# Performance work log

Hardware: AMD Instinct MI355X
Metric: run time of the kernel (lower is better)

Reference implementation:

```python
import jax, jax.numpy as jnp
import numpy as np
from functools import partial

L, B, E, H, NL = 512, 16, 768, 12, 12
D = E // H  # head dim = 64
FF = 4 * E
LN_EPS = 1e-5


def gelu_new(x):
    # HF openai-gpt ACT_FNS['gelu'] (tanh approximation)
    c = np.sqrt(2.0 / np.pi).astype(np.float32)
    return 0.5 * x * (1.0 + jnp.tanh(c * (x + 0.044715 * x * x * x)))


def layer_norm(x, g, b):
    mu = jnp.mean(x, axis=-1, keepdims=True)
    var = jnp.mean(jnp.square(x - mu), axis=-1, keepdims=True)
    return (x - mu) * jax.lax.rsqrt(var + LN_EPS) * g + b


def setup_inputs() -> dict:
    key = jax.random.key(0)
    ks = jax.random.split(key, 8)
    s = 0.02
    x = jax.random.normal(ks[0], (L, B, E), dtype=jnp.float32)
    custom_mask = jnp.ones((B, L), dtype=jnp.float32)
    pos_emb = s * jax.random.normal(ks[1], (L, E), dtype=jnp.float32)
    # stacked per-layer params (leading axis = layer)
    params = {
        'c_attn_w': s * jax.random.normal(ks[2], (NL, E, 3 * E), dtype=jnp.float32),
        'c_attn_b': jnp.zeros((NL, 3 * E), dtype=jnp.float32),
        'attn_proj_w': s * jax.random.normal(ks[3], (NL, E, E), dtype=jnp.float32),
        'attn_proj_b': jnp.zeros((NL, E), dtype=jnp.float32),
        'ln1_g': jnp.ones((NL, E), dtype=jnp.float32),
        'ln1_b': jnp.zeros((NL, E), dtype=jnp.float32),
        'c_fc_w': s * jax.random.normal(ks[4], (NL, E, FF), dtype=jnp.float32),
        'c_fc_b': jnp.zeros((NL, FF), dtype=jnp.float32),
        'mlp_proj_w': s * jax.random.normal(ks[5], (NL, FF, E), dtype=jnp.float32),
        'mlp_proj_b': jnp.zeros((NL, E), dtype=jnp.float32),
        'ln2_g': jnp.ones((NL, E), dtype=jnp.float32),
        'ln2_b': jnp.zeros((NL, E), dtype=jnp.float32),
    }
    return {'x': x, 'custom_mask': custom_mask, 'pos_emb': pos_emb, **params}


def _gpt_forward(x, custom_mask, pos_emb, c_attn_w, c_attn_b, attn_proj_w,
                 attn_proj_b, ln1_g, ln1_b, c_fc_w, c_fc_b, mlp_proj_w,
                 mlp_proj_b, ln2_g, ln2_b):
    Lx, Bx, Ex = x.shape
    h = x.transpose(1, 0, 2) + pos_emb[None, :Lx]  # (B, L, E); dropout = eval identity
    # additive padding mask: (1 - m) * finfo.min, broadcast over heads/queries
    add_mask = (1.0 - custom_mask)[:, None, None, :] * jnp.finfo(jnp.float32).min
    causal = jnp.tril(jnp.ones((Lx, Lx), dtype=jnp.float32))  # bias buffer b

    def block(h, p):
        (caw, cab, apw, apb, g1, b1, fw, fb, pw, pb, g2, b2) = p
        qkv = h @ caw + cab                              # (B, L, 3E)
        q, k, v = jnp.split(qkv, 3, axis=-1)
        q = q.reshape(Bx, Lx, H, D).transpose(0, 2, 1, 3)  # (B, H, L, D)
        k = k.reshape(Bx, Lx, H, D).transpose(0, 2, 1, 3)
        v = v.reshape(Bx, Lx, H, D).transpose(0, 2, 1, 3)
        w = jnp.einsum('bhqd,bhkd->bhqk', q, k) / np.float32(np.sqrt(D))
        w = w * causal + (-10000.0) * (1.0 - causal)     # causal bias masking
        w = w + add_mask
        a = jax.nn.softmax(w, axis=-1)
        o = jnp.einsum('bhqk,bhkd->bhqd', a, v)          # (B, H, L, D)
        o = o.transpose(0, 2, 1, 3).reshape(Bx, Lx, Ex)
        a_out = o @ apw + apb
        n = layer_norm(h + a_out, g1, b1)
        m = gelu_new(n @ fw + fb) @ pw + pb
        h2 = layer_norm(n + m, g2, b2)
        return h2, None

    params = (c_attn_w, c_attn_b, attn_proj_w, attn_proj_b, ln1_g, ln1_b,
              c_fc_w, c_fc_b, mlp_proj_w, mlp_proj_b, ln2_g, ln2_b)
    h, _ = jax.lax.scan(block, h, params)
    return h.transpose(1, 0, 2)  # back to (L, B, E)


def reference(x, custom_mask, pos_emb, c_attn_w, c_attn_b, attn_proj_w,
              attn_proj_b, ln1_g, ln1_b, c_fc_w, c_fc_b, mlp_proj_w,
              mlp_proj_b, ln2_g, ln2_b):
    return _gpt_forward(x, custom_mask, pos_emb, c_attn_w, c_attn_b,
                        attn_proj_w, attn_proj_b, ln1_g, ln1_b, c_fc_w,
                        c_fc_b, mlp_proj_w, mlp_proj_b, ln2_g, ln2_b)
```

## Files before the change

### kernel.cpp

```cpp
#include <hip/hip_runtime.h>
#include <cstdint>
#include <cstddef>


#define LSEQ 512
#define NBATCH 16
#define EDIM 768
#define NHEAD 12
#define NLAYER 12

typedef __attribute__((ext_vector_type(8))) short short8;
typedef __attribute__((ext_vector_type(4))) short short4v;
typedef __attribute__((ext_vector_type(4))) float f32x4;

__device__ __forceinline__ short f2bf(float f) {
  union { float f; unsigned u; } x; x.f = f;
  return (short)((x.u + 0x7FFFu + ((x.u >> 16) & 1u)) >> 16);
}
__device__ __forceinline__ float bf2f(short s) {
  union { unsigned u; float f; } x; x.u = ((unsigned)(unsigned short)s) << 16;
  return x.f;
}

__device__ __forceinline__ void gload_lds16(const void* g, void* l) {
  __builtin_amdgcn_global_load_lds(
      (__attribute__((address_space(1))) void*)(void*)g,
      (__attribute__((address_space(3))) void*)l, 16, 0, 0);
}

__global__ __launch_bounds__(256) void wt_transpose(const float* __restrict__ W,
                                                    short* __restrict__ Wt,
                                                    int K, int N) {
  __shared__ float tile[32][33];
  const int n0 = blockIdx.x * 32, k0 = blockIdx.y * 32;
  const size_t lo = (size_t)blockIdx.z * K * N;
  const float* Ws = W + lo;
  short* Wd = Wt + lo;
  const int tx = threadIdx.x & 31, ty = threadIdx.x >> 5;
#pragma unroll
  for (int i = 0; i < 4; ++i)
    tile[ty + i * 8][tx] = Ws[(size_t)(k0 + ty + i * 8) * N + n0 + tx];
  __syncthreads();
#pragma unroll
  for (int i = 0; i < 4; ++i)
    Wd[(size_t)(n0 + ty + i * 8) * K + k0 + tx] = f2bf(tile[tx][ty + i * 8]);
}

__global__ __launch_bounds__(256) void embed_k(const float* __restrict__ x,
                                               const float* __restrict__ pos,
                                               float* __restrict__ h,
                                               short* __restrict__ hbf) {
  const int row = blockIdx.x;
  const int b = row >> 9, lp = row & 511;
  const int t = threadIdx.x;
#pragma unroll
  for (int i = 0; i < 3; ++i) {
    const int e = t + i * 256;
    float v = x[(size_t)(lp * 16 + b) * 768 + e] + pos[(size_t)lp * 768 + e];
    h[(size_t)row * 768 + e] = v;
    hbf[(size_t)row * 768 + e] = f2bf(v);
  }
}

template <int FINAL>
__global__ __launch_bounds__(256) void ln_fused(const float* __restrict__ A,
                                                const short* __restrict__ B0,
                                                const short* __restrict__ B1,
                                                const float* __restrict__ g,
                                                const float* __restrict__ be,
                                                float* __restrict__ outf,
                                                short* __restrict__ outb) {
  const int row = blockIdx.x * 4 + (threadIdx.x >> 6);
  const int l = threadIdx.x & 63;
  const size_t base = (size_t)row * 768;
  float v[12];
  float s1 = 0.f, s2 = 0.f;
#pragma unroll
  for (int j = 0; j < 3; ++j) {
    const int e = j * 256 + l * 4;
    f32x4 a = *(const f32x4*)&A[base + e];
    short4v b0 = *(const short4v*)&B0[base + e];
    short4v b1 = *(const short4v*)&B1[base + e];
#pragma unroll
    for (int q = 0; q < 4; ++q) {
      float x = a[q] + bf2f(b0[q]) + bf2f(b1[q]);
      v[j * 4 + q] = x; s1 += x; s2 += x * x;
    }
  }
#pragma unroll
  for (int m = 1; m < 64; m <<= 1) {
    s1 += __shfl_xor(s1, m);
    s2 += __shfl_xor(s2, m);
  }
  const float mu = s1 * (1.f / 768.f);
  const float rs = rsqrtf(s2 * (1.f / 768.f) - mu * mu + 1e-5f);
  size_t obase = base;
  if constexpr (FINAL) {
    const int b = row >> 9, lp = row & 511;
    obase = (size_t)(lp * 16 + b) * 768;
  }
#pragma unroll
  for (int j = 0; j < 3; ++j) {
    const int e = j * 256 + l * 4;
    f32x4 gv = *(const f32x4*)&g[e];
    f32x4 bv = *(const f32x4*)&be[e];
    f32x4 of; short4v ob;
#pragma unroll
    for (int q = 0; q < 4; ++q) {
      float o = (v[j * 4 + q] - mu) * rs * gv[q] + bv[q];
      of[q] = o; ob[q] = f2bf(o);
    }
    *(f32x4*)&outf[obase + e] = of;
    if constexpr (!FINAL) *(short4v*)&outb[obase + e] = ob;
  }
}

template <int EPI>
__global__ __launch_bounds__(256) void gemm256(const short* __restrict__ A,
                                               const short* __restrict__ Bt,
                                               const float* __restrict__ bias,
                                               short* __restrict__ C,
                                               int N, int K) {
  constexpr int BK = 64;
  __shared__ alignas(16) short Alds[64 * BK];
  __shared__ alignas(16) short Blds[256 * BK];
  const int t = threadIdx.x;
  const int w = t >> 6, l = t & 63;
  const int wc = w;
  const int l15 = l & 15, lhi = l >> 4;
  const int rowA0 = blockIdx.x * 64;
  const int rowB0 = blockIdx.y * 256;

  f32x4 acc[4][4];
#pragma unroll
  for (int mi = 0; mi < 4; ++mi)
#pragma unroll
    for (int ni = 0; ni < 4; ++ni) acc[mi][ni] = (f32x4){0.f, 0.f, 0.f, 0.f};

  const int srl = w * 8 + (l >> 3);
  const int ss = l & 7;

  const short* aptr[2];
#pragma unroll
  for (int i = 0; i < 2; ++i) {
    const int r = i * 32 + srl;
    aptr[i] = A + (size_t)(rowA0 + r) * K + ((ss ^ (r & 7)) << 3);
  }
  const short* bptr[8];
#pragma unroll
  for (int i = 0; i < 8; ++i) {
    const int r = i * 32 + srl;
    bptr[i] = Bt + (size_t)(rowB0 + r) * K + ((ss ^ (r & 7)) << 3);
  }

  for (int kt = 0; kt < K; kt += BK) {
#pragma unroll
    for (int i = 0; i < 2; ++i) {
      gload_lds16(aptr[i], &Alds[(i * 32 + w * 8) * BK]);
      aptr[i] += BK;
    }
#pragma unroll
    for (int i = 0; i < 8; ++i) {
      gload_lds16(bptr[i], &Blds[(i * 32 + w * 8) * BK]);
      bptr[i] += BK;
    }
    __syncthreads();
    short8 af[4][2], bfr[4][2];
#pragma unroll
    for (int mi = 0; mi < 4; ++mi) {
      const int r = mi * 16 + l15;
#pragma unroll
      for (int kc = 0; kc < 2; ++kc)
        af[mi][kc] = *(const short8*)
            &Alds[r * BK + ((((kc << 2) | lhi) ^ (r & 7)) << 3)];
    }
#pragma unroll
    for (int ni = 0; ni < 4; ++ni) {
      const int r = wc * 64 + ni * 16 + l15;
#pragma unroll
      for (int kc = 0; kc < 2; ++kc)
        bfr[ni][kc] = *(const short8*)
            &Blds[r * BK + ((((kc << 2) | lhi) ^ (r & 7)) << 3)];
    }
#pragma unroll
    for (int mi = 0; mi < 4; ++mi)
#pragma unroll
      for (int ni = 0; ni < 4; ++ni)
#pragma unroll
        for (int kc = 0; kc < 2; ++kc)
          acc[mi][ni] = __builtin_amdgcn_mfma_f32_16x16x32_bf16(
              af[mi][kc], bfr[ni][kc], acc[mi][ni], 0, 0, 0);
    __syncthreads();
  }

  float bv[4];
#pragma unroll
  for (int ni = 0; ni < 4; ++ni) bv[ni] = bias[rowB0 + wc * 64 + ni * 16 + l15];
#pragma unroll
  for (int mi = 0; mi < 4; ++mi) {
#pragma unroll
    for (int ni = 0; ni < 4; ++ni) {
      const int col = rowB0 + wc * 64 + ni * 16 + l15;
#pragma unroll
      for (int i = 0; i < 4; ++i) {
        const int row = rowA0 + mi * 16 + lhi * 4 + i;
        float v = acc[mi][ni][i] + bv[ni];
        if constexpr (EPI == 1) {
          C[(size_t)row * N + col] = f2bf(v);
        } else {
          float pz = v * fmaf(0.044715f, v * v, 1.0f);
          float e = __expf(-1.5957691216057308f * pz);
          float r = __builtin_amdgcn_rcpf(1.0f + e);
          C[(size_t)row * N + col] = f2bf(v * r);
        }
      }
    }
  }
}

__global__ __launch_bounds__(256) void gemm_pk(const short* __restrict__ A,
                                               const short* __restrict__ Bt,
                                               const float* __restrict__ bias,
                                               short* __restrict__ C,
                                               int N, int Kfull) {
  constexpr int BK = 64;
  __shared__ alignas(16) short Alds[128 * BK];
  __shared__ alignas(16) short Blds[128 * BK];
  const int t = threadIdx.x;
  const int w = t >> 6, l = t & 63;
  const int wr = w >> 1, wc = w & 1;
  const int l15 = l & 15, lhi = l >> 4;
  const int rowA0 = blockIdx.x * 128;
  const int rowB0 = blockIdx.y * 128;
  const int z = blockIdx.z;
  const int Ks = Kfull >> 1;
  const int koff = z * Ks;
  short* Cp = C + (size_t)z * 8192 * N;

  f32x4 acc[4][4];
#pragma unroll
  for (int mi = 0; mi < 4; ++mi)
#pragma unroll
    for (int ni = 0; ni < 4; ++ni) acc[mi][ni] = (f32x4){0.f, 0.f, 0.f, 0.f};

  const int srl = l >> 3;
  const int ss = l & 7;

  const short* aptr[4];
  const short* bptr[4];
#pragma unroll
  for (int i = 0; i < 4; ++i) {
    const int r = i * 32 + w * 8 + srl;
    aptr[i] = A + (size_t)(rowA0 + r) * Kfull + koff + ((ss ^ (r & 7)) << 3);
    bptr[i] = Bt + (size_t)(rowB0 + r) * Kfull + koff + ((ss ^ (r & 7)) << 3);
  }

  for (int kt = 0; kt < Ks; kt += BK) {
#pragma unroll
    for (int i = 0; i < 4; ++i) {
      gload_lds16(aptr[i], &Alds[i * 2048 + w * 512]);
      gload_lds16(bptr[i], &Blds[i * 2048 + w * 512]);
      aptr[i] += BK; bptr[i] += BK;
    }
    __syncthreads();
    short8 af[4][2], bfr[4][2];
#pragma unroll
    for (int mi = 0; mi < 4; ++mi) {
      const int r = wr * 64 + mi * 16 + l15;
#pragma unroll
      for (int kc = 0; kc < 2; ++kc)
        af[mi][kc] = *(const short8*)
            &Alds[r * 64 + ((((kc << 2) | lhi) ^ (r & 7)) << 3)];
    }
#pragma unroll
    for (int ni = 0; ni < 4; ++ni) {
      const int r = wc * 64 + ni * 16 + l15;
#pragma unroll
      for (int kc = 0; kc < 2; ++kc)
        bfr[ni][kc] = *(const short8*)
            &Blds[r * 64 + ((((kc << 2) | lhi) ^ (r & 7)) << 3)];
    }
#pragma unroll
    for (int mi = 0; mi < 4; ++mi)
#pragma unroll
      for (int ni = 0; ni < 4; ++ni)
#pragma unroll
        for (int kc = 0; kc < 2; ++kc)
          acc[mi][ni] = __builtin_amdgcn_mfma_f32_16x16x32_bf16(
              af[mi][kc], bfr[ni][kc], acc[mi][ni], 0, 0, 0);
    __syncthreads();
  }

  float bv[4];
#pragma unroll
  for (int ni = 0; ni < 4; ++ni)
    bv[ni] = (z == 0) ? bias[rowB0 + wc * 64 + ni * 16 + l15] : 0.f;
#pragma unroll
  for (int mi = 0; mi < 4; ++mi) {
#pragma unroll
    for (int ni = 0; ni < 4; ++ni) {
      const int col = rowB0 + wc * 64 + ni * 16 + l15;
#pragma unroll
      for (int i = 0; i < 4; ++i) {
        const int row = rowA0 + wr * 64 + mi * 16 + lhi * 4 + i;
        Cp[(size_t)row * N + col] = f2bf(acc[mi][ni][i] + bv[ni]);
      }
    }
  }
}

__global__ __launch_bounds__(256) void attn_k(const short* __restrict__ qkv,
                                              const float* __restrict__ mask,
                                              short* __restrict__ o) {
  const int qb = blockIdx.x;
  const int hh = blockIdx.y;
  const int b = blockIdx.z;
  const int t = threadIdx.x, w = t >> 6, l = t & 63;
  const int l15 = l & 15, lhi = l >> 4;
  __shared__ alignas(16) short Klds[64 * 64];
  __shared__ alignas(16) short Vlds[64 * 64];
  __shared__ alignas(16) short Plds[4][16 * 72];

  short8 qa[2];
  {
    const size_t base =
        (size_t)(b * LSEQ + qb * 64 + w * 16 + l15) * 2304 + hh * 64;
    qa[0] = *(const short8*)&qkv[base + lhi * 8];
    qa[1] = *(const short8*)&qkv[base + 32 + lhi * 8];
  }
  float mrow[4] = {-1e30f, -1e30f, -1e30f, -1e30f};
  float lrow[4] = {0.f, 0.f, 0.f, 0.f};
  const f32x4 zero4 = {0.f, 0.f, 0.f, 0.f};
  f32x4 oacc[4];
#pragma unroll
  for (int nt = 0; nt < 4; ++nt) oacc[nt] = zero4;

  const int nkt = qb + 1;
  for (int kt = 0; kt < nkt; ++kt) {
    __syncthreads();
    {
      const int kr = t >> 2, cc = (t & 3) * 16;
      const size_t grow = (size_t)(b * LSEQ + kt * 64 + kr) * 2304 + hh * 64;
      short8 k0 = *(const short8*)&qkv[grow + 768 + cc];
      short8 k1 = *(const short8*)&qkv[grow + 768 + cc + 8];
      short8 v0 = *(const short8*)&qkv[grow + 1536 + cc];
      short8 v1 = *(const short8*)&qkv[grow + 1536 + cc + 8];
      const int sw = (kr & 7) << 4;
      *(short8*)((char*)Klds + ((kr * 128 + cc * 2) ^ sw)) = k0;
      *(short8*)((char*)Klds + ((kr * 128 + cc * 2 + 16) ^ sw)) = k1;
#pragma unroll
      for (int e = 0; e < 8; ++e) {
        const int n0 = cc + e, n1 = cc + 8 + e;
        ((short*)Vlds)[((n0 * 128 + kr * 2) ^ ((n0 & 7) << 4)) >> 1] = v0[e];
        ((short*)Vlds)[((n1 * 128 + kr * 2) ^ ((n1 & 7) << 4)) >> 1] = v1[e];
      }
    }
    __syncthreads();

    f32x4 s[4];
#pragma unroll
    for (int jt = 0; jt < 4; ++jt) {
      f32x4 z = zero4;
#pragma unroll
      for (int kc = 0; kc < 2; ++kc) {
        const int rowk = jt * 16 + l15;
        short8 kb = *(const short8*)((char*)Klds +
                     ((rowk * 128 + kc * 64 + lhi * 16) ^ ((rowk & 7) << 4)));
        z = __builtin_amdgcn_mfma_f32_16x16x32_bf16(qa[kc], kb, z, 0, 0, 0);
      }
      s[jt] = z;
    }

    float addm[4];
#pragma unroll
    for (int jt = 0; jt < 4; ++jt)
      addm[jt] = (1.0f - mask[b * LSEQ + kt * 64 + jt * 16 + l15]) *
                 -3.402823466e38f;
#pragma unroll
    for (int jt = 0; jt < 4; ++jt) {
      const int colg = kt * 64 + jt * 16 + l15;
#pragma unroll
      for (int i = 0; i < 4; ++i) {
        const int rowg = qb * 64 + w * 16 + lhi * 4 + i;
        float sv = s[jt][i] * 0.125f;
        if (colg > rowg) sv = -10000.0f;
        s[jt][i] = sv + addm[jt];
      }
    }

    float mnew[4], sc[4];
#pragma unroll
    for (int i = 0; i < 4; ++i) {
      float tm = fmaxf(fmaxf(s[0][i], s[1][i]), fmaxf(s[2][i], s[3][i]));
#pragma unroll
      for (int mm = 1; mm < 16; mm <<= 1) tm = fmaxf(tm, __shfl_xor(tm, mm));
      mnew[i] = fmaxf(mrow[i], tm);
      sc[i] = __expf(mrow[i] - mnew[i]);
      mrow[i] = mnew[i];
    }
#pragma unroll
    for (int i = 0; i < 4; ++i) {
      float ts = 0.f;
#pragma unroll
      for (int jt = 0; jt < 4; ++jt) {
        float p = __expf(s[jt][i] - mnew[i]);
        s[jt][i] = p;
        ts += p;
      }
#pragma unroll
      for (int mm = 1; mm < 16; mm <<= 1) ts += __shfl_xor(ts, mm);
      lrow[i] = lrow[i] * sc[i] + ts;
      oacc[0][i] *= sc[i]; oacc[1][i] *= sc[i];
      oacc[2][i] *= sc[i]; oacc[3][i] *= sc[i];
    }

    short* Pw = &Plds[w][0];
#pragma unroll
    for (int jt = 0; jt < 4; ++jt)
#pragma unroll
      for (int i = 0; i < 4; ++i)
        Pw[(lhi * 4 + i) * 72 + jt * 16 + l15] = f2bf(s[jt][i]);
    __syncthreads();
    short8 pa[2];
#pragma unroll
    for (int kc = 0; kc < 2; ++kc)
      pa[kc] = *(const short8*)&Pw[l15 * 72 + kc * 32 + lhi * 8];

#pragma unroll
    for (int nt = 0; nt < 4; ++nt) {
#pragma unroll
      for (int kc = 0; kc < 2; ++kc) {
        const int rown = nt * 16 + l15;
        short8 vb = *(const short8*)((char*)Vlds +
                     ((rown * 128 + kc * 64 + lhi * 16) ^ ((rown & 7) << 4)));
        oacc[nt] = __builtin_amdgcn_mfma_f32_16x16x32_bf16(pa[kc], vb,
                                                           oacc[nt], 0, 0, 0);
      }
    }
  }

#pragma unroll
  for (int i = 0; i < 4; ++i) {
    const size_t row = (size_t)(b * LSEQ + qb * 64 + w * 16 + lhi * 4 + i);
    const float inv = 1.0f / lrow[i];
#pragma unroll
    for (int nt = 0; nt < 4; ++nt)
      o[row * 768 + hh * 64 + nt * 16 + l15] = f2bf(oacc[nt][i] * inv);
  }
}

extern "C" void kernel_launch(void* const* d_in, const int* in_sizes, int n_in,
                              void* d_out, int out_size, void* d_ws,
                              size_t ws_size, hipStream_t stream) {
  const float* x    = (const float*)d_in[0];
  const float* mask = (const float*)d_in[1];
  const float* pos  = (const float*)d_in[2];
  const float* caw  = (const float*)d_in[3];
  const float* cab  = (const float*)d_in[4];
  const float* apw  = (const float*)d_in[5];
  const float* apb  = (const float*)d_in[6];
  const float* g1   = (const float*)d_in[7];
  const float* b1   = (const float*)d_in[8];
  const float* fw   = (const float*)d_in[9];
  const float* fb   = (const float*)d_in[10];
  const float* pw   = (const float*)d_in[11];
  const float* pb   = (const float*)d_in[12];
  const float* g2   = (const float*)d_in[13];
  const float* b2   = (const float*)d_in[14];

  char* ws = (char*)d_ws;
  size_t off = 0;
  auto alloc = [&](size_t bytes) {
    size_t o = off;
    off += (bytes + 255) & ~(size_t)255;
    return o;
  };
  float* h    = (float*)(ws + alloc(8192ull * 768 * 4));
  short* hbf  = (short*)(ws + alloc(8192ull * 768 * 2));
  float* nrm  = (float*)(ws + alloc(8192ull * 768 * 4));
  short* nbf  = (short*)(ws + alloc(8192ull * 768 * 2));
  short* qkvb = (short*)(ws + alloc(8192ull * 2304 * 2));
  short* obf  = (short*)(ws + alloc(8192ull * 768 * 2));
  short* aout = (short*)(ws + alloc(2ull * 8192 * 768 * 2));
  short* gbf  = (short*)(ws + alloc(8192ull * 3072 * 2));
  short* wt_attn = (short*)(ws + alloc(12ull * 768 * 2304 * 2));
  short* wt_proj = (short*)(ws + alloc(12ull * 768 * 768 * 2));
  short* wt_fc   = (short*)(ws + alloc(12ull * 768 * 3072 * 2));
  short* wt_mlp  = (short*)(ws + alloc(12ull * 3072 * 768 * 2));
  short* aout1 = aout + 8192ull * 768;
  (void)ws_size; (void)in_sizes; (void)n_in; (void)out_size;

  wt_transpose<<<dim3(2304 / 32, 768 / 32, 12), 256, 0, stream>>>(caw, wt_attn, 768, 2304);
  wt_transpose<<<dim3(768 / 32, 768 / 32, 12), 256, 0, stream>>>(apw, wt_proj, 768, 768);
  wt_transpose<<<dim3(3072 / 32, 768 / 32, 12), 256, 0, stream>>>(fw, wt_fc, 768, 3072);
  wt_transpose<<<dim3(768 / 32, 3072 / 32, 12), 256, 0, stream>>>(pw, wt_mlp, 3072, 768);

  embed_k<<<8192, 256, 0, stream>>>(x, pos, h, hbf);

  for (int L = 0; L < 12; ++L) {
    gemm256<1><<<dim3(128, 9), 256, 0, stream>>>(
        hbf, wt_attn + (size_t)L * 2304 * 768, cab + (size_t)L * 2304, qkvb, 2304, 768);
    attn_k<<<dim3(8, 12, 16), 256, 0, stream>>>(qkvb, mask, obf);
    gemm_pk<<<dim3(64, 6, 2), 256, 0, stream>>>(
        obf, wt_proj + (size_t)L * 768 * 768, apb + (size_t)L * 768, aout, 768, 768);
    ln_fused<0><<<2048, 256, 0, stream>>>(h, aout, aout1, g1 + (size_t)L * 768,
                                          b1 + (size_t)L * 768, nrm, nbf);
    gemm256<2><<<dim3(128, 12), 256, 0, stream>>>(
        nbf, wt_fc + (size_t)L * 768 * 3072, fb + (size_t)L * 3072, gbf, 3072, 768);
    gemm_pk<<<dim3(64, 6, 2), 256, 0, stream>>>(
        gbf, wt_mlp + (size_t)L * 3072 * 768, pb + (size_t)L * 768, aout, 768, 3072);
    if (L < 11) {
      ln_fused<0><<<2048, 256, 0, stream>>>(nrm, aout, aout1, g2 + (size_t)L * 768,
                                            b2 + (size_t)L * 768, h, hbf);
    } else {
      ln_fused<1><<<2048, 256, 0, stream>>>(nrm, aout, aout1, g2 + (size_t)L * 768,
                                            b2 + (size_t)L * 768, (float*)d_out,
                                            nullptr);
    }
  }
}
```

Measured before the change: 3.247 ms.

## Drop fp32 residual stream, write V transposed from QKV GEMM, widen FC GEMM

The fp32 copies of the residual stream (h, nrm) are removed. LayerNorm now reads its residual input as bf16 and writes only bf16, or fp32 only for the final output. The QKV GEMM epilogue writes V transposed into a separate buffer, so attention can load K and V tiles straight into LDS with async loads instead of scattering V element by element. The FC+GELU GEMM moves to a 512-thread 128x256 tile kernel. These cut memory traffic and LDS work, at the cost of bf16 rounding of the residual across layers and uncoalesced stores for the transposed V.

```diff
diff --git a/kernel.cpp b/kernel.cpp
--- a/kernel.cpp
+++ b/kernel.cpp
@@ -48,7 +48,6 @@
 
 __global__ __launch_bounds__(256) void embed_k(const float* __restrict__ x,
                                                const float* __restrict__ pos,
-                                               float* __restrict__ h,
                                                short* __restrict__ hbf) {
   const int row = blockIdx.x;
   const int b = row >> 9, lp = row & 511;
@@ -57,19 +56,17 @@
   for (int i = 0; i < 3; ++i) {
     const int e = t + i * 256;
     float v = x[(size_t)(lp * 16 + b) * 768 + e] + pos[(size_t)lp * 768 + e];
-    h[(size_t)row * 768 + e] = v;
     hbf[(size_t)row * 768 + e] = f2bf(v);
   }
 }
 
 template <int FINAL>
-__global__ __launch_bounds__(256) void ln_fused(const float* __restrict__ A,
+__global__ __launch_bounds__(256) void ln_fused(const short* __restrict__ A,
                                                 const short* __restrict__ B0,
                                                 const short* __restrict__ B1,
                                                 const float* __restrict__ g,
                                                 const float* __restrict__ be,
-                                                float* __restrict__ outf,
-                                                short* __restrict__ outb) {
+                                                void* __restrict__ out) {
   const int row = blockIdx.x * 4 + (threadIdx.x >> 6);
   const int l = threadIdx.x & 63;
   const size_t base = (size_t)row * 768;
@@ -78,12 +75,12 @@
 #pragma unroll
   for (int j = 0; j < 3; ++j) {
     const int e = j * 256 + l * 4;
-    f32x4 a = *(const f32x4*)&A[base + e];
+    short4v a = *(const short4v*)&A[base + e];
     short4v b0 = *(const short4v*)&B0[base + e];
     short4v b1 = *(const short4v*)&B1[base + e];
 #pragma unroll
     for (int q = 0; q < 4; ++q) {
-      float x = a[q] + bf2f(b0[q]) + bf2f(b1[q]);
+      float x = bf2f(a[q]) + bf2f(b0[q]) + bf2f(b1[q]);
       v[j * 4 + q] = x; s1 += x; s2 += x * x;
     }
   }
@@ -104,23 +101,28 @@
     const int e = j * 256 + l * 4;
     f32x4 gv = *(const f32x4*)&g[e];
     f32x4 bv = *(const f32x4*)&be[e];
-    f32x4 of; short4v ob;
-#pragma unroll
-    for (int q = 0; q < 4; ++q) {
-      float o = (v[j * 4 + q] - mu) * rs * gv[q] + bv[q];
-      of[q] = o; ob[q] = f2bf(o);
-    }
-    *(f32x4*)&outf[obase + e] = of;
-    if constexpr (!FINAL) *(short4v*)&outb[obase + e] = ob;
-  }
-}
-
-template <int EPI>
-__global__ __launch_bounds__(256) void gemm256(const short* __restrict__ A,
-                                               const short* __restrict__ Bt,
-                                               const float* __restrict__ bias,
-                                               short* __restrict__ C,
-                                               int N, int K) {
+    if constexpr (FINAL) {
+      f32x4 of;
+#pragma unroll
+      for (int q = 0; q < 4; ++q)
+        of[q] = (v[j * 4 + q] - mu) * rs * gv[q] + bv[q];
+      *(f32x4*)&((float*)out)[obase + e] = of;
+    } else {
+      short4v ob;
+#pragma unroll
+      for (int q = 0; q < 4; ++q)
+        ob[q] = f2bf((v[j * 4 + q] - mu) * rs * gv[q] + bv[q]);
+      *(short4v*)&((short*)out)[obase + e] = ob;
+    }
+  }
+}
+
+__global__ __launch_bounds__(256) void gemm_qkv(const short* __restrict__ A,
+                                                const short* __restrict__ Bt,
+                                                const float* __restrict__ bias,
+                                                short* __restrict__ C,
+                                                short* __restrict__ Vt,
+                                                int N, int K) {
   constexpr int BK = 64;
   __shared__ alignas(16) short Alds[64 * BK];
   __shared__ alignas(16) short Blds[256 * BK];
@@ -193,6 +195,7 @@
     __syncthreads();
   }
 
+  const bool isV = (rowB0 >= 1536);
   float bv[4];
 #pragma unroll
   for (int ni = 0; ni < 4; ++ni) bv[ni] = bias[rowB0 + wc * 64 + ni * 16 + l15];
@@ -204,15 +207,107 @@
 #pragma unroll
       for (int i = 0; i < 4; ++i) {
         const int row = rowA0 + mi * 16 + lhi * 4 + i;
+        const short s = f2bf(acc[mi][ni][i] + bv[ni]);
+        if (!isV) C[(size_t)row * N + col] = s;
+        else      Vt[(size_t)(col - 1536) * 8192 + row] = s;
+      }
+    }
+  }
+}
+
+__global__ __launch_bounds__(512) void gemm512(const short* __restrict__ A,
+                                               const short* __restrict__ Bt,
+                                               const float* __restrict__ bias,
+                                               short* __restrict__ C,
+                                               int N, int K) {
+  constexpr int BK = 64;
+  __shared__ alignas(16) short Alds[128 * BK];
+  __shared__ alignas(16) short Blds[256 * BK];
+  const int t = threadIdx.x;
+  const int w = t >> 6, l = t & 63;
+  const int wr = w >> 2, wc = w & 3;
+  const int l15 = l & 15, lhi = l >> 4;
+  const int rowA0 = blockIdx.x * 128;
+  const int rowB0 = blockIdx.y * 256;
+
+  f32x4 acc[4][4];
+#pragma unroll
+  for (int mi = 0; mi < 4; ++mi)
+#pragma unroll
+    for (int ni = 0; ni < 4; ++ni) acc[mi][ni] = (f32x4){0.f, 0.f, 0.f, 0.f};
+
+  const int srl = w * 8 + (l >> 3);
+  const int ss = l & 7;
+
+  const short* aptr[2];
+#pragma unroll
+  for (int i = 0; i < 2; ++i) {
+    const int r = i * 64 + srl;
+    aptr[i] = A + (size_t)(rowA0 + r) * K + ((ss ^ (r & 7)) << 3);
+  }
+  const short* bptr[4];
+#pragma unroll
+  for (int i = 0; i < 4; ++i) {
+    const int r = i * 64 + srl;
+    bptr[i] = Bt + (size_t)(rowB0 + r) * K + ((ss ^ (r & 7)) << 3);
+  }
+
+  for (int kt = 0; kt < K; kt += BK) {
+#pragma unroll
+    for (int i = 0; i < 2; ++i) {
+      gload_lds16(aptr[i], &Alds[(i * 64 + w * 8) * BK]);
+      aptr[i] += BK;
+    }
+#pragma unroll
+    for (int i = 0; i < 4; ++i) {
+      gload_lds16(bptr[i], &Blds[(i * 64 + w * 8) * BK]);
+      bptr[i] += BK;
+    }
+    __syncthreads();
+    short8 af[4][2], bfr[4][2];
+#pragma unroll
+    for (int mi = 0; mi < 4; ++mi) {
+      const int r = wr * 64 + mi * 16 + l15;
+#pragma unroll
+      for (int kc = 0; kc < 2; ++kc)
+        af[mi][kc] = *(const short8*)
+            &Alds[r * BK + ((((kc << 2) | lhi) ^ (r & 7)) << 3)];
+    }
+#pragma unroll
+    for (int ni = 0; ni < 4; ++ni) {
+      const int r = wc * 64 + ni * 16 + l15;
+#pragma unroll
+      for (int kc = 0; kc < 2; ++kc)
+        bfr[ni][kc] = *(const short8*)
+            &Blds[r * BK + ((((kc << 2) | lhi) ^ (r & 7)) << 3)];
+    }
+#pragma unroll
+    for (int mi = 0; mi < 4; ++mi)
+#pragma unroll
+      for (int ni = 0; ni < 4; ++ni)
+#pragma unroll
+        for (int kc = 0; kc < 2; ++kc)
+          acc[mi][ni] = __builtin_amdgcn_mfma_f32_16x16x32_bf16(
+              af[mi][kc], bfr[ni][kc], acc[mi][ni], 0, 0, 0);
+    __syncthreads();
+  }
+
+  float bv[4];
+#pragma unroll
+  for (int ni = 0; ni < 4; ++ni) bv[ni] = bias[rowB0 + wc * 64 + ni * 16 + l15];
+#pragma unroll
+  for (int mi = 0; mi < 4; ++mi) {
+#pragma unroll
+    for (int ni = 0; ni < 4; ++ni) {
+      const int col = rowB0 + wc * 64 + ni * 16 + l15;
+#pragma unroll
+      for (int i = 0; i < 4; ++i) {
+        const int row = rowA0 + wr * 64 + mi * 16 + lhi * 4 + i;
         float v = acc[mi][ni][i] + bv[ni];
-        if constexpr (EPI == 1) {
-          C[(size_t)row * N + col] = f2bf(v);
-        } else {
-          float pz = v * fmaf(0.044715f, v * v, 1.0f);
-          float e = __expf(-1.5957691216057308f * pz);
-          float r = __builtin_amdgcn_rcpf(1.0f + e);
-          C[(size_t)row * N + col] = f2bf(v * r);
-        }
+        float pz = v * fmaf(0.044715f, v * v, 1.0f);
+        float e = __expf(-1.5957691216057308f * pz);
+        float r = __builtin_amdgcn_rcpf(1.0f + e);
+        C[(size_t)row * N + col] = f2bf(v * r);
       }
     }
   }
@@ -310,6 +405,7 @@
 }
 
 __global__ __launch_bounds__(256) void attn_k(const short* __restrict__ qkv,
+                                              const short* __restrict__ Vt,
                                               const float* __restrict__ mask,
                                               short* __restrict__ o) {
   const int qb = blockIdx.x;
@@ -319,7 +415,6 @@
   const int l15 = l & 15, lhi = l >> 4;
   __shared__ alignas(16) short Klds[64 * 64];
   __shared__ alignas(16) short Vlds[64 * 64];
-  __shared__ alignas(16) short Plds[4][16 * 72];
 
   short8 qa[2];
   {
@@ -328,6 +423,7 @@
     qa[0] = *(const short8*)&qkv[base + lhi * 8];
     qa[1] = *(const short8*)&qkv[base + 32 + lhi * 8];
   }
+  __shared__ alignas(16) short Plds[4][16 * 72];
   float mrow[4] = {-1e30f, -1e30f, -1e30f, -1e30f};
   float lrow[4] = {0.f, 0.f, 0.f, 0.f};
   const f32x4 zero4 = {0.f, 0.f, 0.f, 0.f};
@@ -335,25 +431,19 @@
 #pragma unroll
   for (int nt = 0; nt < 4; ++nt) oacc[nt] = zero4;
 
+  const int lr = l >> 3, sl = l & 7;
   const int nkt = qb + 1;
   for (int kt = 0; kt < nkt; ++kt) {
     __syncthreads();
-    {
-      const int kr = t >> 2, cc = (t & 3) * 16;
-      const size_t grow = (size_t)(b * LSEQ + kt * 64 + kr) * 2304 + hh * 64;
-      short8 k0 = *(const short8*)&qkv[grow + 768 + cc];
-      short8 k1 = *(const short8*)&qkv[grow + 768 + cc + 8];
-      short8 v0 = *(const short8*)&qkv[grow + 1536 + cc];
-      short8 v1 = *(const short8*)&qkv[grow + 1536 + cc + 8];
-      const int sw = (kr & 7) << 4;
-      *(short8*)((char*)Klds + ((kr * 128 + cc * 2) ^ sw)) = k0;
-      *(short8*)((char*)Klds + ((kr * 128 + cc * 2 + 16) ^ sw)) = k1;
-#pragma unroll
-      for (int e = 0; e < 8; ++e) {
-        const int n0 = cc + e, n1 = cc + 8 + e;
-        ((short*)Vlds)[((n0 * 128 + kr * 2) ^ ((n0 & 7) << 4)) >> 1] = v0[e];
-        ((short*)Vlds)[((n1 * 128 + kr * 2) ^ ((n1 & 7) << 4)) >> 1] = v1[e];
-      }
+#pragma unroll
+    for (int i = 0; i < 2; ++i) {
+      const int kr = i * 32 + w * 8 + lr;
+      gload_lds16(qkv + (size_t)(b * LSEQ + kt * 64 + kr) * 2304 + 768 +
+                      hh * 64 + ((sl ^ (kr & 7)) << 3),
+                  &Klds[(i * 32 + w * 8) * 64]);
+      gload_lds16(Vt + (size_t)(hh * 64 + kr) * 8192 + b * LSEQ + kt * 64 +
+                      ((sl ^ (kr & 7)) << 3),
+                  &Vlds[(i * 32 + w * 8) * 64]);
     }
     __syncthreads();
 
@@ -475,11 +565,10 @@
     off += (bytes + 255) & ~(size_t)255;
     return o;
   };
-  float* h    = (float*)(ws + alloc(8192ull * 768 * 4));
   short* hbf  = (short*)(ws + alloc(8192ull * 768 * 2));
-  float* nrm  = (float*)(ws + alloc(8192ull * 768 * 4));
   short* nbf  = (short*)(ws + alloc(8192ull * 768 * 2));
   short* qkvb = (short*)(ws + alloc(8192ull * 2304 * 2));
+  short* vT   = (short*)(ws + alloc(768ull * 8192 * 2));
   short* obf  = (short*)(ws + alloc(8192ull * 768 * 2));
   short* aout = (short*)(ws + alloc(2ull * 8192 * 768 * 2));
   short* gbf  = (short*)(ws + alloc(8192ull * 3072 * 2));
@@ -495,27 +584,27 @@
   wt_transpose<<<dim3(3072 / 32, 768 / 32, 12), 256, 0, stream>>>(fw, wt_fc, 768, 3072);
   wt_transpose<<<dim3(768 / 32, 3072 / 32, 12), 256, 0, stream>>>(pw, wt_mlp, 3072, 768);
 
-  embed_k<<<8192, 256, 0, stream>>>(x, pos, h, hbf);
+  embed_k<<<8192, 256, 0, stream>>>(x, pos, hbf);
 
   for (int L = 0; L < 12; ++L) {
-    gemm256<1><<<dim3(128, 9), 256, 0, stream>>>(
-        hbf, wt_attn + (size_t)L * 2304 * 768, cab + (size_t)L * 2304, qkvb, 2304, 768);
-    attn_k<<<dim3(8, 12, 16), 256, 0, stream>>>(qkvb, mask, obf);
+    gemm_qkv<<<dim3(128, 9), 256, 0, stream>>>(
+        hbf, wt_attn + (size_t)L * 2304 * 768, cab + (size_t)L * 2304, qkvb,
+        vT, 2304, 768);
+    attn_k<<<dim3(8, 12, 16), 256, 0, stream>>>(qkvb, vT, mask, obf);
     gemm_pk<<<dim3(64, 6, 2), 256, 0, stream>>>(
         obf, wt_proj + (size_t)L * 768 * 768, apb + (size_t)L * 768, aout, 768, 768);
-    ln_fused<0><<<2048, 256, 0, stream>>>(h, aout, aout1, g1 + (size_t)L * 768,
-                                          b1 + (size_t)L * 768, nrm, nbf);
-    gemm256<2><<<dim3(128, 12), 256, 0, stream>>>(
+    ln_fused<0><<<2048, 256, 0, stream>>>(hbf, aout, aout1, g1 + (size_t)L * 768,
+                                          b1 + (size_t)L * 768, nbf);
+    gemm512<<<dim3(64, 12), 512, 0, stream>>>(
         nbf, wt_fc + (size_t)L * 768 * 3072, fb + (size_t)L * 3072, gbf, 3072, 768);
     gemm_pk<<<dim3(64, 6, 2), 256, 0, stream>>>(
         gbf, wt_mlp + (size_t)L * 3072 * 768, pb + (size_t)L * 768, aout, 768, 3072);
     if (L < 11) {
-      ln_fused<0><<<2048, 256, 0, stream>>>(nrm, aout, aout1, g2 + (size_t)L * 768,
-                                            b2 + (size_t)L * 768, h, hbf);
+      ln_fused<0><<<2048, 256, 0, stream>>>(nbf, aout, aout1, g2 + (size_t)L * 768,
+                                            b2 + (size_t)L * 768, hbf);
     } else {
-      ln_fused<1><<<2048, 256, 0, stream>>>(nrm, aout, aout1, g2 + (size_t)L * 768,
-                                            b2 + (size_t)L * 768, (float*)d_out,
-                                            nullptr);
-    }
-  }
-}
+      ln_fused<1><<<2048, 256, 0, stream>>>(nbf, aout, aout1, g2 + (size_t)L * 768,
+                                            b2 + (size_t)L * 768, (float*)d_out);
+    }
+  }
+}
```

New measurement: 3.195 ms. About the same (-1.6%).
